# Kernel optimization log

Hardware: AMD Instinct MI355X
Metric: run time of the kernel (lower is better)

The kernel has to match this reference:

```python
import jax, jax.numpy as jnp
import numpy as np

N, E, C0, H, NC = 50000, 800000, 64, 64, 2500
NUM_LAYERS = 3


def setup_inputs() -> dict:
    key = jax.random.key(0)
    ks = jax.random.split(key, 16)
    inp = {}
    inp["x"] = jax.random.normal(ks[0], (N, C0), dtype=jnp.float32)
    inp["edge_index"] = jax.random.randint(ks[1], (2, E), 0, N, dtype=jnp.int64)
    inp["cluster"] = jax.random.randint(ks[2], (N,), 0, NC, dtype=jnp.int64)
    c = C0
    for i in range(NUM_LAYERS):
        inp[f"w1_{i}"] = jax.random.normal(ks[3 + 4 * i], (c, H), jnp.float32) / np.sqrt(c).astype(np.float32)
        inp[f"b1_{i}"] = jnp.zeros((H,), jnp.float32)
        inp[f"w2_{i}"] = jax.random.normal(ks[4 + 4 * i], (H, c), jnp.float32) / np.sqrt(H).astype(np.float32)
        inp[f"b2_{i}"] = jnp.zeros((c,), jnp.float32)
        c *= 2
    inp["n_clusters"] = NC
    return inp


def _glp(x, src, dst, w1, b1, w2, b2, num_nodes):
    # node encoder MLP: Linear -> ReLU -> Linear
    h = jnp.maximum(x @ w1 + b1, 0.0) @ w2 + b2  # [N, c]
    # message passing: gather at source, scatter-max at destination
    msg = h[src]  # [E, c]
    aggr = jax.ops.segment_max(msg, dst, num_segments=num_nodes)  # [N, c]
    # nodes with no incoming edges -> 0 (PyG fill for max aggregation)
    aggr = jnp.where(jnp.isfinite(aggr), aggr, 0.0)
    # update: concat(encoder_out, aggregated) -> channels double
    return jnp.concatenate([h, aggr], axis=1)


def reference(x, edge_index, cluster,
              w1_0, b1_0, w2_0, b2_0,
              w1_1, b1_1, w2_1, b2_1,
              w1_2, b1_2, w2_2, b2_2,
              n_clusters):
    num_nodes = x.shape[0]
    src, dst = edge_index[0], edge_index[1]
    params = [(w1_0, b1_0, w2_0, b2_0), (w1_1, b1_1, w2_1, b2_1), (w1_2, b1_2, w2_2, b2_2)]
    for (w1, b1, w2, b2) in params:
        x = _glp(x, src, dst, w1, b1, w2, b2, num_nodes)
    # cluster-wise max pool over polylines
    pooled = jax.ops.segment_max(x, cluster, num_segments=n_clusters)  # [NC, 512]
    pooled = jnp.where(jnp.isfinite(pooled), pooled, 0.0)
    # column-wise (dim=0) normalization as in the source
    out = pooled / (jnp.linalg.norm(pooled, axis=0) + 1e-6)
    return out
```

## Files before the change

### kernel.cpp

```cpp
#include <hip/hip_runtime.h>
#include <math.h>

typedef unsigned short bfu;
typedef __attribute__((ext_vector_type(8))) short bf16x8;
typedef __attribute__((ext_vector_type(16))) float f32x16;

__device__ __forceinline__ float b2f(bfu u) {
    unsigned int x = ((unsigned int)u) << 16;
    return __uint_as_float(x);
}
__device__ __forceinline__ bfu f2bf(float f) {
    unsigned int u = __float_as_uint(f);
    unsigned int r = (u + 0x7FFFu + ((u >> 16) & 1u)) >> 16;
    return (bfu)r;
}

struct InitArgs {
    int* deg; int N; int* cdeg; int NC; float* sumsq;
    const float* w[6]; bfu* whi[6]; bfu* wlo[6]; int K[6]; int Nw[6];
    const float* x0; bfu* xhi; bfu* xlo; int xtotal;
};

__global__ __launch_bounds__(256) void k_init(InitArgs a) {
    const int j = blockIdx.y;
    const int g0 = blockIdx.x * 256 + threadIdx.x;
    const int gs = gridDim.x * 256;
    if (j == 0) {
        for (int i = g0; i < a.N; i += gs) a.deg[i] = 0;
        for (int i = g0; i < a.NC; i += gs) a.cdeg[i] = 0;
        for (int i = g0; i < 512; i += gs) a.sumsq[i] = 0.f;
    } else if (j <= 6) {
        const int jj = j - 1;
        const int K = a.K[jj], Nw = a.Nw[jj];
        const int total = K * Nw;
        const float* w = a.w[jj];
        bfu* dhi = a.whi[jj];
        bfu* dlo = a.wlo[jj];
        for (int idx = g0; idx < total; idx += gs) {
            int k = idx / Nw, n = idx % Nw;
            float v = w[idx];
            bfu hi = f2bf(v);
            bfu lo = f2bf(v - b2f(hi));
            dhi[n * K + k] = hi;
            dlo[n * K + k] = lo;
        }
    } else {
        for (int i = g0; i * 4 < a.xtotal; i += gs) {
            int base = i * 4;
            float4 v = *(const float4*)&a.x0[base];
            ushort4 h, l;
            h.x = f2bf(v.x); l.x = f2bf(v.x - b2f(h.x));
            h.y = f2bf(v.y); l.y = f2bf(v.y - b2f(h.y));
            h.z = f2bf(v.z); l.z = f2bf(v.z - b2f(h.z));
            h.w = f2bf(v.w); l.w = f2bf(v.w - b2f(h.w));
            *(ushort4*)&a.xhi[base] = h;
            *(ushort4*)&a.xlo[base] = l;
        }
    }
}

__global__ void k_hist2(const int* __restrict__ dst, int E, int* __restrict__ deg,
                        const int* __restrict__ cluster, int N, int* __restrict__ cdeg) {
    int i = blockIdx.x * blockDim.x + threadIdx.x;
    if (i < E) atomicAdd(&deg[dst[i]], 1);
    if (i < N) atomicAdd(&cdeg[cluster[i]], 1);
}

__global__ __launch_bounds__(256) void k_scanA(const int* __restrict__ deg, int N,
                                               const int* __restrict__ cdeg, int NC,
                                               int* __restrict__ scn0, int* __restrict__ scn1,
                                               int* __restrict__ bsum0, int* __restrict__ bsum1) {
    __shared__ int part[256];
    const int seg = blockIdx.y;
    const int n = seg ? NC : N;
    const int* d = seg ? cdeg : deg;
    int* scn = seg ? scn1 : scn0;
    int* bs  = seg ? bsum1 : bsum0;
    const int b = blockIdx.x;
    if (b * 256 >= n) return;
    const int t = threadIdx.x;
    const int i = b * 256 + t;
    int v = (i < n) ? d[i] : 0;
    part[t] = v;
    __syncthreads();
#pragma unroll
    for (int off = 1; off < 256; off <<= 1) {
        int cv = part[t];
        int u = (t >= off) ? part[t - off] : 0;
        __syncthreads();
        part[t] = cv + u;
        __syncthreads();
    }
    if (i < n) scn[i] = part[t];
    if (t == 255) bs[b] = part[255];
}

__global__ __launch_bounds__(256) void k_scanC(const int* __restrict__ deg, int N,
                                               const int* __restrict__ cdeg, int NC,
                                               const int* __restrict__ scn0, const int* __restrict__ scn1,
                                               const int* __restrict__ bsum0, int nb0,
                                               const int* __restrict__ bsum1, int nb1,
                                               int* __restrict__ ptr0, int* __restrict__ cur0,
                                               int* __restrict__ ptr1, int* __restrict__ cur1) {
    __shared__ int part[256];
    const int seg = blockIdx.y;
    const int n = seg ? NC : N;
    const int nb = seg ? nb1 : nb0;
    const int* d = seg ? cdeg : deg;
    const int* scn = seg ? scn1 : scn0;
    const int* bsum = seg ? bsum1 : bsum0;
    int* ptr = seg ? ptr1 : ptr0;
    int* cur = seg ? cur1 : cur0;
    const int b = blockIdx.x;
    if (b * 256 >= n) return;
    const int t = threadIdx.x;
    int v = (t < nb) ? bsum[t] : 0;
    part[t] = v;
    __syncthreads();
#pragma unroll
    for (int off = 1; off < 256; off <<= 1) {
        int cv = part[t];
        int u = (t >= off) ? part[t - off] : 0;
        __syncthreads();
        part[t] = cv + u;
        __syncthreads();
    }
    const int boff = (b == 0) ? 0 : part[b - 1];
    const int i = b * 256 + t;
    if (i < n) {
        int e = boff + scn[i] - d[i];
        ptr[i] = e;
        cur[i] = e;
    }
    if (b == 0 && t == 0) ptr[n] = part[nb - 1];
}

__global__ void k_scatter2(const int* __restrict__ dst, const int* __restrict__ src, int E,
                           int* __restrict__ cur, int* __restrict__ colidx,
                           const int* __restrict__ cluster, int N,
                           int* __restrict__ ccur, int* __restrict__ cidx) {
    int i = blockIdx.x * blockDim.x + threadIdx.x;
    if (i < E) {
        int d = dst[i];
        int pos = atomicAdd(&cur[d], 1);
        colidx[pos] = src[i];
    }
    if (i < N) {
        int c = cluster[i];
        int pos = atomicAdd(&ccur[c], 1);
        cidx[pos] = i;
    }
}

__device__ __forceinline__ int swz(int row, int kb) {
    return (row * 128 + (kb ^ ((row & 7) << 4))) >> 1;
}

template <bool WLO>
__global__ __launch_bounds__(256) void k_layer(const bfu* __restrict__ Ahi, const bfu* __restrict__ Alo,
                                               const bfu* __restrict__ W1hi, const bfu* __restrict__ W1lo,
                                               const float* __restrict__ b1,
                                               const bfu* __restrict__ W2hi, const bfu* __restrict__ W2lo,
                                               const float* __restrict__ b2,
                                               bfu* __restrict__ Ohi, bfu* __restrict__ Olo,
                                               int M, int K, int Kzero, int Nw2, int OS) {
    __shared__ __align__(16) bfu As[2][128 * 64];
    __shared__ __align__(16) bfu Bs[2][64 * 64];
    const int tid = threadIdx.x;
    const int wave = tid >> 6, lane = tid & 63;
    const int m0 = blockIdx.x * 128;
    const int l31 = lane & 31;
    const int khalfb = (lane >> 5) * 16;
    const int arow = wave * 32 + l31;

    f32x16 acc0, acc1;
#pragma unroll
    for (int i = 0; i < 16; i++) { acc0[i] = 0.f; acc1[i] = 0.f; }

    for (int k0 = 0; k0 < K; k0 += 64) {
        const bool full3 = (k0 < Kzero);
#pragma unroll
        for (int i = 0; i < 4; i++) {
            int idx = i * 2048 + tid * 8;
            int row = idx >> 6;
            int ke = idx & 63;
            int gm = m0 + row; if (gm >= M) gm = M - 1;
            uint4 v = *(const uint4*)&Ahi[(size_t)gm * K + k0 + ke];
            *(uint4*)&As[0][swz(row, ke * 2)] = v;
        }
        if (full3) {
#pragma unroll
            for (int i = 0; i < 4; i++) {
                int idx = i * 2048 + tid * 8;
                int row = idx >> 6;
                int ke = idx & 63;
                int gm = m0 + row; if (gm >= M) gm = M - 1;
                uint4 v = *(const uint4*)&Alo[(size_t)gm * K + k0 + ke];
                *(uint4*)&As[1][swz(row, ke * 2)] = v;
            }
        }
#pragma unroll
        for (int p = 0; p < 2; p++) {
            const bfu* src = p ? W1lo : W1hi;
#pragma unroll
            for (int i = 0; i < 2; i++) {
                int idx = i * 2048 + tid * 8;
                int row = idx >> 6;
                int ke = idx & 63;
                uint4 v = *(const uint4*)&src[(size_t)row * K + k0 + ke];
                *(uint4*)&Bs[p][swz(row, ke * 2)] = v;
            }
        }
        __syncthreads();
#pragma unroll
        for (int s = 0; s < 4; s++) {
            int kb = s * 32 + khalfb;
            bf16x8 ah = *(const bf16x8*)&As[0][swz(arow, kb)];
            bf16x8 bh0 = *(const bf16x8*)&Bs[0][swz(l31, kb)];
            bf16x8 bl0 = *(const bf16x8*)&Bs[1][swz(l31, kb)];
            bf16x8 bh1 = *(const bf16x8*)&Bs[0][swz(32 + l31, kb)];
            bf16x8 bl1 = *(const bf16x8*)&Bs[1][swz(32 + l31, kb)];
            acc0 = __builtin_amdgcn_mfma_f32_32x32x16_bf16(ah, bh0, acc0, 0, 0, 0);
            acc0 = __builtin_amdgcn_mfma_f32_32x32x16_bf16(ah, bl0, acc0, 0, 0, 0);
            acc1 = __builtin_amdgcn_mfma_f32_32x32x16_bf16(ah, bh1, acc1, 0, 0, 0);
            acc1 = __builtin_amdgcn_mfma_f32_32x32x16_bf16(ah, bl1, acc1, 0, 0, 0);
            if (full3) {
                bf16x8 al = *(const bf16x8*)&As[1][swz(arow, kb)];
                acc0 = __builtin_amdgcn_mfma_f32_32x32x16_bf16(al, bh0, acc0, 0, 0, 0);
                acc1 = __builtin_amdgcn_mfma_f32_32x32x16_bf16(al, bh1, acc1, 0, 0, 0);
            }
        }
        __syncthreads();
    }

    {
        float bc0 = b1[l31];
        float bc1 = b1[32 + l31];
        const int rbase = wave * 32 + 4 * (lane >> 5);
#pragma unroll
        for (int r = 0; r < 16; r++) {
            int row = rbase + (r & 3) + 8 * (r >> 2);
            float t0 = fmaxf(acc0[r] + bc0, 0.f);
            float t1 = fmaxf(acc1[r] + bc1, 0.f);
            bfu h0 = f2bf(t0), h1 = f2bf(t1);
            bfu l0 = f2bf(t0 - b2f(h0)), l1 = f2bf(t1 - b2f(h1));
            As[0][swz(row, l31 * 2)] = h0;
            As[0][swz(row, (32 + l31) * 2)] = h1;
            As[1][swz(row, l31 * 2)] = l0;
            As[1][swz(row, (32 + l31) * 2)] = l1;
        }
    }

    for (int n0 = 0; n0 < Nw2; n0 += 64) {
        __syncthreads();
#pragma unroll
        for (int p = 0; p < 2; p++) {
            const bfu* src = p ? W2lo : W2hi;
#pragma unroll
            for (int i = 0; i < 2; i++) {
                int idx = i * 2048 + tid * 8;
                int row = idx >> 6;
                int ke = idx & 63;
                uint4 v = *(const uint4*)&src[(size_t)(n0 + row) * 64 + ke];
                *(uint4*)&Bs[p][swz(row, ke * 2)] = v;
            }
        }
        __syncthreads();
#pragma unroll
        for (int i = 0; i < 16; i++) { acc0[i] = 0.f; acc1[i] = 0.f; }
#pragma unroll
        for (int s = 0; s < 4; s++) {
            int kb = s * 32 + khalfb;
            bf16x8 th = *(const bf16x8*)&As[0][swz(arow, kb)];
            bf16x8 tl = *(const bf16x8*)&As[1][swz(arow, kb)];
            bf16x8 wh0 = *(const bf16x8*)&Bs[0][swz(l31, kb)];
            bf16x8 wl0 = *(const bf16x8*)&Bs[1][swz(l31, kb)];
            bf16x8 wh1 = *(const bf16x8*)&Bs[0][swz(32 + l31, kb)];
            bf16x8 wl1 = *(const bf16x8*)&Bs[1][swz(32 + l31, kb)];
            acc0 = __builtin_amdgcn_mfma_f32_32x32x16_bf16(th, wh0, acc0, 0, 0, 0);
            acc0 = __builtin_amdgcn_mfma_f32_32x32x16_bf16(th, wl0, acc0, 0, 0, 0);
            acc0 = __builtin_amdgcn_mfma_f32_32x32x16_bf16(tl, wh0, acc0, 0, 0, 0);
            acc1 = __builtin_amdgcn_mfma_f32_32x32x16_bf16(th, wh1, acc1, 0, 0, 0);
            acc1 = __builtin_amdgcn_mfma_f32_32x32x16_bf16(th, wl1, acc1, 0, 0, 0);
            acc1 = __builtin_amdgcn_mfma_f32_32x32x16_bf16(tl, wh1, acc1, 0, 0, 0);
        }
        float bc0 = b2[n0 + l31];
        float bc1 = b2[n0 + 32 + l31];
        const int rbase = m0 + wave * 32 + 4 * (lane >> 5);
#pragma unroll
        for (int r = 0; r < 16; r++) {
            int grow = rbase + (r & 3) + 8 * (r >> 2);
            if (grow < M) {
                float o0 = acc0[r] + bc0;
                float o1 = acc1[r] + bc1;
                bfu h0 = f2bf(o0), h1 = f2bf(o1);
                size_t base = (size_t)grow * OS + n0;
                Ohi[base + l31] = h0;
                Ohi[base + 32 + l31] = h1;
                if (WLO) {
                    Olo[base + l31] = f2bf(o0 - b2f(h0));
                    Olo[base + 32 + l31] = f2bf(o1 - b2f(h1));
                }
            }
        }
    }
}

template <int R>
__device__ __forceinline__ void gmax(const bfu* __restrict__ p, float* acc) {
    if (R == 4) {
        ushort4 v = *(const ushort4*)p;
        acc[0] = fmaxf(acc[0], b2f(v.x)); acc[1] = fmaxf(acc[1], b2f(v.y));
        acc[2] = fmaxf(acc[2], b2f(v.z)); acc[3] = fmaxf(acc[3], b2f(v.w));
    } else if (R == 2) {
        ushort2 v = *(const ushort2*)p;
        acc[0] = fmaxf(acc[0], b2f(v.x)); acc[1] = fmaxf(acc[1], b2f(v.y));
    } else {
        acc[0] = fmaxf(acc[0], b2f(*p));
    }
}

template <int R>
__global__ void k_agg(const bfu* __restrict__ hplane, bfu* __restrict__ whi,
                      const int* __restrict__ rowptr, const int* __restrict__ colidx,
                      int N, int stride) {
    const int wid = (blockIdx.x * blockDim.x + threadIdx.x) >> 6;
    const int lane = threadIdx.x & 63;
    if (wid >= N) return;
    const int beg = rowptr[wid], end = rowptr[wid + 1];
    const int ch = lane * R;

    float acc[R];
#pragma unroll
    for (int r = 0; r < R; r++) acc[r] = -INFINITY;

    int i = beg;
    for (; i + 8 <= end; i += 8) {
        int off[8];
#pragma unroll
        for (int u = 0; u < 8; u++) off[u] = colidx[i + u] * stride + ch;
#pragma unroll
        for (int u = 0; u < 8; u++) gmax<R>(hplane + off[u], acc);
    }
    for (; i + 2 <= end; i += 2) {
        int o0 = colidx[i] * stride + ch;
        int o1 = colidx[i + 1] * stride + ch;
        gmax<R>(hplane + o0, acc);
        gmax<R>(hplane + o1, acc);
    }
    if (i < end) gmax<R>(hplane + colidx[i] * stride + ch, acc);

    if (beg == end) {
#pragma unroll
        for (int r = 0; r < R; r++) acc[r] = 0.f;
    }
    int obase = wid * stride + 64 * R + ch;
#pragma unroll
    for (int r = 0; r < R; r++) whi[obase + r] = f2bf(acc[r]);
}

__global__ void k_pool(const bfu* __restrict__ xhi,
                       const int* __restrict__ cptr, const int* __restrict__ cidx,
                       float* __restrict__ pooled) {
    int cl = blockIdx.x;
    int tid = threadIdx.x;
    int beg = cptr[cl], end = cptr[cl + 1];
    float ax = -INFINITY, ay = -INFINITY;
    int i = beg;
    for (; i + 4 <= end; i += 4) {
        ushort2 h0 = *(const ushort2*)&xhi[cidx[i + 0] * 512 + tid * 2];
        ushort2 h1 = *(const ushort2*)&xhi[cidx[i + 1] * 512 + tid * 2];
        ushort2 h2 = *(const ushort2*)&xhi[cidx[i + 2] * 512 + tid * 2];
        ushort2 h3 = *(const ushort2*)&xhi[cidx[i + 3] * 512 + tid * 2];
        ax = fmaxf(ax, fmaxf(fmaxf(b2f(h0.x), b2f(h1.x)), fmaxf(b2f(h2.x), b2f(h3.x))));
        ay = fmaxf(ay, fmaxf(fmaxf(b2f(h0.y), b2f(h1.y)), fmaxf(b2f(h2.y), b2f(h3.y))));
    }
    for (; i < end; i++) {
        ushort2 h = *(const ushort2*)&xhi[cidx[i] * 512 + tid * 2];
        ax = fmaxf(ax, b2f(h.x)); ay = fmaxf(ay, b2f(h.y));
    }
    if (beg == end) { ax = 0.f; ay = 0.f; }
    float2 o; o.x = ax; o.y = ay;
    *(float2*)&pooled[(size_t)cl * 512 + tid * 2] = o;
}

__global__ void k_sumsq(const float* __restrict__ pooled, float* __restrict__ sumsq, int NC) {
    int tid = threadIdx.x;
    float ax = 0.f, ay = 0.f;
    for (int r = blockIdx.x; r < NC; r += gridDim.x) {
        float2 v = *(const float2*)&pooled[(size_t)r * 512 + tid * 2];
        ax += v.x * v.x; ay += v.y * v.y;
    }
    atomicAdd(&sumsq[tid * 2 + 0], ax);
    atomicAdd(&sumsq[tid * 2 + 1], ay);
}

__global__ void k_scale(const float* __restrict__ pooled, const float* __restrict__ sumsq,
                        float* __restrict__ out, int total) {
    int i = blockIdx.x * blockDim.x + threadIdx.x;
    int base = i * 4;
    if (base < total) {
        float4 v = *(const float4*)&pooled[base];
        int col = base & 511;
        v.x /= (sqrtf(sumsq[col + 0]) + 1e-6f);
        v.y /= (sqrtf(sumsq[col + 1]) + 1e-6f);
        v.z /= (sqrtf(sumsq[col + 2]) + 1e-6f);
        v.w /= (sqrtf(sumsq[col + 3]) + 1e-6f);
        *(float4*)&out[base] = v;
    }
}

extern "C" void kernel_launch(void* const* d_in, const int* in_sizes, int n_in,
                              void* d_out, int out_size, void* d_ws, size_t ws_size,
                              hipStream_t stream) {
    const float* x0      = (const float*)d_in[0];
    const int*   ei      = (const int*)d_in[1];
    const int*   cluster = (const int*)d_in[2];
    const float* w1_[3] = {(const float*)d_in[3], (const float*)d_in[7],  (const float*)d_in[11]};
    const float* b1_[3] = {(const float*)d_in[4], (const float*)d_in[8],  (const float*)d_in[12]};
    const float* w2_[3] = {(const float*)d_in[5], (const float*)d_in[9],  (const float*)d_in[13]};
    const float* b2_[3] = {(const float*)d_in[6], (const float*)d_in[10], (const float*)d_in[14]};

    const int N  = in_sizes[2];
    const int E  = in_sizes[1] / 2;
    const int NC = 2500;
    float* out = (float*)d_out;

    char* p = (char*)d_ws;
    auto alloc = [&](size_t bytes) -> char* {
        char* r = p;
        p += (bytes + 255) & ~(size_t)255;
        return r;
    };
    bfu* X0hi = (bfu*)alloc((size_t)N * 64 * 2);
    bfu* X0lo = (bfu*)alloc((size_t)N * 64 * 2);
    bfu* X1hi = (bfu*)alloc((size_t)N * 128 * 2);
    bfu* X1lo = (bfu*)alloc((size_t)N * 128 * 2);
    bfu* X2hi = (bfu*)alloc((size_t)N * 256 * 2);
    bfu* X2lo = (bfu*)alloc((size_t)N * 256 * 2);
    bfu* X3hi = (bfu*)alloc((size_t)N * 512 * 2);
    bfu* w1t_hi[3]; bfu* w1t_lo[3]; bfu* w2t_hi[3]; bfu* w2t_lo[3];
    const int Ks[3] = {64, 128, 256};
    for (int l = 0; l < 3; l++) {
        w1t_hi[l] = (bfu*)alloc((size_t)64 * Ks[l] * 2);
        w1t_lo[l] = (bfu*)alloc((size_t)64 * Ks[l] * 2);
        w2t_hi[l] = (bfu*)alloc((size_t)Ks[l] * 64 * 2);
        w2t_lo[l] = (bfu*)alloc((size_t)Ks[l] * 64 * 2);
    }
    float* pooled = (float*)alloc((size_t)NC * 512 * 4);
    float* sumsq  = (float*)alloc(512 * 4);
    int*   deg    = (int*)alloc((size_t)(N + 1) * 4);
    int*   rowptr = (int*)alloc((size_t)(N + 1) * 4);
    int*   cursor = (int*)alloc((size_t)(N + 1) * 4);
    int*   colidx = (int*)alloc((size_t)E * 4);
    int*   cdeg   = (int*)alloc((size_t)(NC + 1) * 4);
    int*   cptr   = (int*)alloc((size_t)(NC + 1) * 4);
    int*   ccur   = (int*)alloc((size_t)(NC + 1) * 4);
    int*   cidx   = (int*)alloc((size_t)N * 4);
    int*   scn0   = (int*)alloc((size_t)N * 4);
    int*   scn1   = (int*)alloc((size_t)NC * 4);
    int*   bsum0  = (int*)alloc(256 * 4);
    int*   bsum1  = (int*)alloc(256 * 4);

    const int* src = ei;
    const int* dst = ei + E;

    InitArgs ia;
    ia.deg = deg; ia.N = N; ia.cdeg = cdeg; ia.NC = NC; ia.sumsq = sumsq;
    for (int l = 0; l < 3; l++) {
        ia.w[2 * l]     = w1_[l]; ia.whi[2 * l]     = w1t_hi[l]; ia.wlo[2 * l]     = w1t_lo[l];
        ia.K[2 * l]     = Ks[l];  ia.Nw[2 * l]      = 64;
        ia.w[2 * l + 1] = w2_[l]; ia.whi[2 * l + 1] = w2t_hi[l]; ia.wlo[2 * l + 1] = w2t_lo[l];
        ia.K[2 * l + 1] = 64;     ia.Nw[2 * l + 1]  = Ks[l];
    }
    ia.x0 = x0; ia.xhi = X0hi; ia.xlo = X0lo; ia.xtotal = N * 64;
    k_init<<<dim3(128, 8), 256, 0, stream>>>(ia);

    k_hist2<<<(E + 255) / 256, 256, 0, stream>>>(dst, E, deg, cluster, N, cdeg);

    const int nb0 = (N + 255) / 256;
    const int nb1 = (NC + 255) / 256;
    k_scanA<<<dim3(nb0, 2), 256, 0, stream>>>(deg, N, cdeg, NC, scn0, scn1, bsum0, bsum1);
    k_scanC<<<dim3(nb0, 2), 256, 0, stream>>>(deg, N, cdeg, NC, scn0, scn1, bsum0, nb0, bsum1, nb1,
                                              rowptr, cursor, cptr, ccur);

    k_scatter2<<<(E + 255) / 256, 256, 0, stream>>>(dst, src, E, cursor, colidx,
                                                    cluster, N, ccur, cidx);

    const int Mt = (N + 127) / 128;
    const int aggBlocks = (N * 64 + 255) / 256;

    k_layer<true><<<Mt, 256, 0, stream>>>(X0hi, X0lo, w1t_hi[0], w1t_lo[0], b1_[0],
                                          w2t_hi[0], w2t_lo[0], b2_[0], X1hi, X1lo,
                                          N, 64, 64, 64, 128);
    k_agg<1><<<aggBlocks, 256, 0, stream>>>(X1hi, X1hi, rowptr, colidx, N, 128);

    k_layer<true><<<Mt, 256, 0, stream>>>(X1hi, X1lo, w1t_hi[1], w1t_lo[1], b1_[1],
                                          w2t_hi[1], w2t_lo[1], b2_[1], X2hi, X2lo,
                                          N, 128, 64, 128, 256);
    k_agg<2><<<aggBlocks, 256, 0, stream>>>(X2hi, X2hi, rowptr, colidx, N, 256);

    k_layer<false><<<Mt, 256, 0, stream>>>(X2hi, X2lo, w1t_hi[2], w1t_lo[2], b1_[2],
                                           w2t_hi[2], w2t_lo[2], b2_[2], X3hi, nullptr,
                                           N, 256, 128, 256, 512);
    k_agg<4><<<aggBlocks, 256, 0, stream>>>(X3hi, X3hi, rowptr, colidx, N, 512);

    k_pool<<<NC, 256, 0, stream>>>(X3hi, cptr, cidx, pooled);
    k_sumsq<<<64, 256, 0, stream>>>(pooled, sumsq, NC);
    k_scale<<<(out_size / 4 + 255) / 256, 256, 0, stream>>>(pooled, sumsq, out, out_size);
}
```

Baseline: 303.5 us.

## Split each wavefront across several edges with 16-byte gathers in aggregation

Rewrites the scatter-max aggregation kernel so each wavefront breaks into sub-groups that each handle a different incoming edge. Every lane loads 8 bf16 channels (16 bytes) at once, and partial maxima are combined across sub-groups with xor shuffles. The aim is fewer, wider memory transactions and more parallel gathers per node, since average degree is about 16. The cost is the shuffle reduction, idle lanes on low-degree nodes, and duplicated loads in the tail.

```diff
diff --git a/kernel.cpp b/kernel.cpp
--- a/kernel.cpp
+++ b/kernel.cpp
@@ -306,57 +306,76 @@
     }
 }
 
-template <int R>
-__device__ __forceinline__ void gmax(const bfu* __restrict__ p, float* acc) {
-    if (R == 4) {
-        ushort4 v = *(const ushort4*)p;
-        acc[0] = fmaxf(acc[0], b2f(v.x)); acc[1] = fmaxf(acc[1], b2f(v.y));
-        acc[2] = fmaxf(acc[2], b2f(v.z)); acc[3] = fmaxf(acc[3], b2f(v.w));
-    } else if (R == 2) {
-        ushort2 v = *(const ushort2*)p;
-        acc[0] = fmaxf(acc[0], b2f(v.x)); acc[1] = fmaxf(acc[1], b2f(v.y));
-    } else {
-        acc[0] = fmaxf(acc[0], b2f(*p));
-    }
-}
-
-template <int R>
-__global__ void k_agg(const bfu* __restrict__ hplane, bfu* __restrict__ whi,
-                      const int* __restrict__ rowptr, const int* __restrict__ colidx,
-                      int N, int stride) {
+__device__ __forceinline__ void gmax8(const bfu* __restrict__ p, float* acc) {
+    uint4 v = *(const uint4*)p;
+    acc[0] = fmaxf(acc[0], __uint_as_float(v.x << 16));
+    acc[1] = fmaxf(acc[1], __uint_as_float(v.x & 0xffff0000u));
+    acc[2] = fmaxf(acc[2], __uint_as_float(v.y << 16));
+    acc[3] = fmaxf(acc[3], __uint_as_float(v.y & 0xffff0000u));
+    acc[4] = fmaxf(acc[4], __uint_as_float(v.z << 16));
+    acc[5] = fmaxf(acc[5], __uint_as_float(v.z & 0xffff0000u));
+    acc[6] = fmaxf(acc[6], __uint_as_float(v.w << 16));
+    acc[7] = fmaxf(acc[7], __uint_as_float(v.w & 0xffff0000u));
+}
+
+template <int LPR, int STRIDE>
+__global__ void k_aggw(const bfu* __restrict__ hplane, bfu* __restrict__ whi,
+                       const int* __restrict__ rowptr, const int* __restrict__ colidx,
+                       int N) {
     const int wid = (blockIdx.x * blockDim.x + threadIdx.x) >> 6;
     const int lane = threadIdx.x & 63;
     if (wid >= N) return;
     const int beg = rowptr[wid], end = rowptr[wid + 1];
-    const int ch = lane * R;
-
-    float acc[R];
-#pragma unroll
-    for (int r = 0; r < R; r++) acc[r] = -INFINITY;
+    constexpr int EPL = 64 / LPR;
+    const int sub = lane >> ( LPR == 32 ? 5 : (LPR == 16 ? 4 : 3) );
+    const int ll  = lane & (LPR - 1);
+    const int ch  = ll * 8;
+
+    float acc[8];
+#pragma unroll
+    for (int r = 0; r < 8; r++) acc[r] = -INFINITY;
 
     int i = beg;
-    for (; i + 8 <= end; i += 8) {
+    for (; i + 8 * EPL <= end; i += 8 * EPL) {
         int off[8];
 #pragma unroll
-        for (int u = 0; u < 8; u++) off[u] = colidx[i + u] * stride + ch;
-#pragma unroll
-        for (int u = 0; u < 8; u++) gmax<R>(hplane + off[u], acc);
-    }
-    for (; i + 2 <= end; i += 2) {
-        int o0 = colidx[i] * stride + ch;
-        int o1 = colidx[i + 1] * stride + ch;
-        gmax<R>(hplane + o0, acc);
-        gmax<R>(hplane + o1, acc);
-    }
-    if (i < end) gmax<R>(hplane + colidx[i] * stride + ch, acc);
+        for (int u = 0; u < 8; u++) off[u] = colidx[i + u * EPL + sub] * STRIDE + ch;
+#pragma unroll
+        for (int u = 0; u < 8; u++) gmax8(hplane + off[u], acc);
+    }
+    for (; i + 2 * EPL <= end; i += 2 * EPL) {
+        int o0 = colidx[i + sub] * STRIDE + ch;
+        int o1 = colidx[i + EPL + sub] * STRIDE + ch;
+        gmax8(hplane + o0, acc);
+        gmax8(hplane + o1, acc);
+    }
+    for (; i + EPL <= end; i += EPL) {
+        gmax8(hplane + colidx[i + sub] * STRIDE + ch, acc);
+    }
+    if (i < end) {
+        int r = end - i;
+        int e = i + (sub < r ? sub : r - 1);
+        gmax8(hplane + colidx[e] * STRIDE + ch, acc);
+    }
+
+#pragma unroll
+    for (int m = LPR; m < 64; m <<= 1) {
+#pragma unroll
+        for (int r = 0; r < 8; r++) acc[r] = fmaxf(acc[r], __shfl_xor(acc[r], m, 64));
+    }
 
     if (beg == end) {
 #pragma unroll
-        for (int r = 0; r < R; r++) acc[r] = 0.f;
-    }
-    int obase = wid * stride + 64 * R + ch;
-#pragma unroll
-    for (int r = 0; r < R; r++) whi[obase + r] = f2bf(acc[r]);
+        for (int r = 0; r < 8; r++) acc[r] = 0.f;
+    }
+    if (sub == 0) {
+        ushort4 w0, w1;
+        w0.x = f2bf(acc[0]); w0.y = f2bf(acc[1]); w0.z = f2bf(acc[2]); w0.w = f2bf(acc[3]);
+        w1.x = f2bf(acc[4]); w1.y = f2bf(acc[5]); w1.z = f2bf(acc[6]); w1.w = f2bf(acc[7]);
+        bfu* q = whi + (size_t)wid * STRIDE + STRIDE / 2 + ch;
+        *(ushort4*)q = w0;
+        *(ushort4*)(q + 4) = w1;
+    }
 }
 
 __global__ void k_pool(const bfu* __restrict__ xhi,
@@ -493,17 +512,17 @@
     k_layer<true><<<Mt, 256, 0, stream>>>(X0hi, X0lo, w1t_hi[0], w1t_lo[0], b1_[0],
                                           w2t_hi[0], w2t_lo[0], b2_[0], X1hi, X1lo,
                                           N, 64, 64, 64, 128);
-    k_agg<1><<<aggBlocks, 256, 0, stream>>>(X1hi, X1hi, rowptr, colidx, N, 128);
+    k_aggw<8, 128><<<aggBlocks, 256, 0, stream>>>(X1hi, X1hi, rowptr, colidx, N);
 
     k_layer<true><<<Mt, 256, 0, stream>>>(X1hi, X1lo, w1t_hi[1], w1t_lo[1], b1_[1],
                                           w2t_hi[1], w2t_lo[1], b2_[1], X2hi, X2lo,
                                           N, 128, 64, 128, 256);
-    k_agg<2><<<aggBlocks, 256, 0, stream>>>(X2hi, X2hi, rowptr, colidx, N, 256);
+    k_aggw<16, 256><<<aggBlocks, 256, 0, stream>>>(X2hi, X2hi, rowptr, colidx, N);
 
     k_layer<false><<<Mt, 256, 0, stream>>>(X2hi, X2lo, w1t_hi[2], w1t_lo[2], b1_[2],
                                            w2t_hi[2], w2t_lo[2], b2_[2], X3hi, nullptr,
                                            N, 256, 128, 256, 512);
-    k_agg<4><<<aggBlocks, 256, 0, stream>>>(X3hi, X3hi, rowptr, colidx, N, 512);
+    k_aggw<32, 512><<<aggBlocks, 256, 0, stream>>>(X3hi, X3hi, rowptr, colidx, N);
 
     k_pool<<<NC, 256, 0, stream>>>(X3hi, cptr, cidx, pooled);
     k_sumsq<<<64, 256, 0, stream>>>(pooled, sumsq, NC);
```

New measurement: 309.2 us. About the same (+1.9%).

## Halve MLP row tile to 64 and split output columns across waves

Applied to the files above, without the earlier changes.

The fused two-layer MLP kernel now processes 64 rows per block instead of 128. The four waves form a 2x2 grid (row half by column half), so each wave holds one 32x32 accumulator instead of two. This halves LDS use for the A tile and the accumulator registers, and doubles the number of blocks, which should raise occupancy and parallelism over the 50k rows. In exchange, the weight tiles are loaded from global memory twice as often per row, and each wave has half as many MFMAs in flight.

```diff
diff --git a/kernel.cpp b/kernel.cpp
--- a/kernel.cpp
+++ b/kernel.cpp
@@ -164,23 +164,24 @@
                                                const float* __restrict__ b2,
                                                bfu* __restrict__ Ohi, bfu* __restrict__ Olo,
                                                int M, int K, int Kzero, int Nw2, int OS) {
-    __shared__ __align__(16) bfu As[2][128 * 64];
+    __shared__ __align__(16) bfu As[2][64 * 64];
     __shared__ __align__(16) bfu Bs[2][64 * 64];
     const int tid = threadIdx.x;
     const int wave = tid >> 6, lane = tid & 63;
-    const int m0 = blockIdx.x * 128;
+    const int m0 = blockIdx.x * 64;
     const int l31 = lane & 31;
     const int khalfb = (lane >> 5) * 16;
-    const int arow = wave * 32 + l31;
-
-    f32x16 acc0, acc1;
-#pragma unroll
-    for (int i = 0; i < 16; i++) { acc0[i] = 0.f; acc1[i] = 0.f; }
+    const int arow = (wave & 1) * 32 + l31;
+    const int cbase = (wave >> 1) * 32;
+
+    f32x16 acc;
+#pragma unroll
+    for (int i = 0; i < 16; i++) acc[i] = 0.f;
 
     for (int k0 = 0; k0 < K; k0 += 64) {
         const bool full3 = (k0 < Kzero);
 #pragma unroll
-        for (int i = 0; i < 4; i++) {
+        for (int i = 0; i < 2; i++) {
             int idx = i * 2048 + tid * 8;
             int row = idx >> 6;
             int ke = idx & 63;
@@ -190,7 +191,7 @@
         }
         if (full3) {
 #pragma unroll
-            for (int i = 0; i < 4; i++) {
+            for (int i = 0; i < 2; i++) {
                 int idx = i * 2048 + tid * 8;
                 int row = idx >> 6;
                 int ke = idx & 63;
@@ -216,38 +217,29 @@
         for (int s = 0; s < 4; s++) {
             int kb = s * 32 + khalfb;
             bf16x8 ah = *(const bf16x8*)&As[0][swz(arow, kb)];
-            bf16x8 bh0 = *(const bf16x8*)&Bs[0][swz(l31, kb)];
-            bf16x8 bl0 = *(const bf16x8*)&Bs[1][swz(l31, kb)];
-            bf16x8 bh1 = *(const bf16x8*)&Bs[0][swz(32 + l31, kb)];
-            bf16x8 bl1 = *(const bf16x8*)&Bs[1][swz(32 + l31, kb)];
-            acc0 = __builtin_amdgcn_mfma_f32_32x32x16_bf16(ah, bh0, acc0, 0, 0, 0);
-            acc0 = __builtin_amdgcn_mfma_f32_32x32x16_bf16(ah, bl0, acc0, 0, 0, 0);
-            acc1 = __builtin_amdgcn_mfma_f32_32x32x16_bf16(ah, bh1, acc1, 0, 0, 0);
-            acc1 = __builtin_amdgcn_mfma_f32_32x32x16_bf16(ah, bl1, acc1, 0, 0, 0);
+            bf16x8 bh = *(const bf16x8*)&Bs[0][swz(cbase + l31, kb)];
+            bf16x8 bl = *(const bf16x8*)&Bs[1][swz(cbase + l31, kb)];
+            acc = __builtin_amdgcn_mfma_f32_32x32x16_bf16(ah, bh, acc, 0, 0, 0);
+            acc = __builtin_amdgcn_mfma_f32_32x32x16_bf16(ah, bl, acc, 0, 0, 0);
             if (full3) {
                 bf16x8 al = *(const bf16x8*)&As[1][swz(arow, kb)];
-                acc0 = __builtin_amdgcn_mfma_f32_32x32x16_bf16(al, bh0, acc0, 0, 0, 0);
-                acc1 = __builtin_amdgcn_mfma_f32_32x32x16_bf16(al, bh1, acc1, 0, 0, 0);
+                acc = __builtin_amdgcn_mfma_f32_32x32x16_bf16(al, bh, acc, 0, 0, 0);
             }
         }
         __syncthreads();
     }
 
     {
-        float bc0 = b1[l31];
-        float bc1 = b1[32 + l31];
-        const int rbase = wave * 32 + 4 * (lane >> 5);
+        float bc = b1[cbase + l31];
+        const int rbase = (wave & 1) * 32 + 4 * (lane >> 5);
 #pragma unroll
         for (int r = 0; r < 16; r++) {
             int row = rbase + (r & 3) + 8 * (r >> 2);
-            float t0 = fmaxf(acc0[r] + bc0, 0.f);
-            float t1 = fmaxf(acc1[r] + bc1, 0.f);
-            bfu h0 = f2bf(t0), h1 = f2bf(t1);
-            bfu l0 = f2bf(t0 - b2f(h0)), l1 = f2bf(t1 - b2f(h1));
-            As[0][swz(row, l31 * 2)] = h0;
-            As[0][swz(row, (32 + l31) * 2)] = h1;
-            As[1][swz(row, l31 * 2)] = l0;
-            As[1][swz(row, (32 + l31) * 2)] = l1;
+            float t0 = fmaxf(acc[r] + bc, 0.f);
+            bfu h0 = f2bf(t0);
+            bfu l0 = f2bf(t0 - b2f(h0));
+            As[0][swz(row, (cbase + l31) * 2)] = h0;
+            As[1][swz(row, (cbase + l31) * 2)] = l0;
         }
     }
 
@@ -267,39 +259,30 @@
         }
         __syncthreads();
 #pragma unroll
-        for (int i = 0; i < 16; i++) { acc0[i] = 0.f; acc1[i] = 0.f; }
+        for (int i = 0; i < 16; i++) acc[i] = 0.f;
 #pragma unroll
         for (int s = 0; s < 4; s++) {
             int kb = s * 32 + khalfb;
             bf16x8 th = *(const bf16x8*)&As[0][swz(arow, kb)];
             bf16x8 tl = *(const bf16x8*)&As[1][swz(arow, kb)];
-            bf16x8 wh0 = *(const bf16x8*)&Bs[0][swz(l31, kb)];
-            bf16x8 wl0 = *(const bf16x8*)&Bs[1][swz(l31, kb)];
-            bf16x8 wh1 = *(const bf16x8*)&Bs[0][swz(32 + l31, kb)];
-            bf16x8 wl1 = *(const bf16x8*)&Bs[1][swz(32 + l31, kb)];
-            acc0 = __builtin_amdgcn_mfma_f32_32x32x16_bf16(th, wh0, acc0, 0, 0, 0);
-            acc0 = __builtin_amdgcn_mfma_f32_32x32x16_bf16(th, wl0, acc0, 0, 0, 0);
-            acc0 = __builtin_amdgcn_mfma_f32_32x32x16_bf16(tl, wh0, acc0, 0, 0, 0);
-            acc1 = __builtin_amdgcn_mfma_f32_32x32x16_bf16(th, wh1, acc1, 0, 0, 0);
-            acc1 = __builtin_amdgcn_mfma_f32_32x32x16_bf16(th, wl1, acc1, 0, 0, 0);
-            acc1 = __builtin_amdgcn_mfma_f32_32x32x16_bf16(tl, wh1, acc1, 0, 0, 0);
-        }
-        float bc0 = b2[n0 + l31];
-        float bc1 = b2[n0 + 32 + l31];
-        const int rbase = m0 + wave * 32 + 4 * (lane >> 5);
+            bf16x8 wh = *(const bf16x8*)&Bs[0][swz(cbase + l31, kb)];
+            bf16x8 wl = *(const bf16x8*)&Bs[1][swz(cbase + l31, kb)];
+            acc = __builtin_amdgcn_mfma_f32_32x32x16_bf16(th, wh, acc, 0, 0, 0);
+            acc = __builtin_amdgcn_mfma_f32_32x32x16_bf16(th, wl, acc, 0, 0, 0);
+            acc = __builtin_amdgcn_mfma_f32_32x32x16_bf16(tl, wh, acc, 0, 0, 0);
+        }
+        float bc = b2[n0 + cbase + l31];
+        const int rbase = m0 + (wave & 1) * 32 + 4 * (lane >> 5);
 #pragma unroll
         for (int r = 0; r < 16; r++) {
             int grow = rbase + (r & 3) + 8 * (r >> 2);
             if (grow < M) {
-                float o0 = acc0[r] + bc0;
-                float o1 = acc1[r] + bc1;
-                bfu h0 = f2bf(o0), h1 = f2bf(o1);
-                size_t base = (size_t)grow * OS + n0;
+                float o0 = acc[r] + bc;
+                bfu h0 = f2bf(o0);
+                size_t base = (size_t)grow * OS + n0 + cbase;
                 Ohi[base + l31] = h0;
-                Ohi[base + 32 + l31] = h1;
                 if (WLO) {
                     Olo[base + l31] = f2bf(o0 - b2f(h0));
-                    Olo[base + 32 + l31] = f2bf(o1 - b2f(h1));
                 }
             }
         }
@@ -487,7 +470,7 @@
     k_scatter2<<<(E + 255) / 256, 256, 0, stream>>>(dst, src, E, cursor, colidx,
                                                     cluster, N, ccur, cidx);
 
-    const int Mt = (N + 127) / 128;
+    const int Mt = (N + 63) / 64;
     const int aggBlocks = (N * 64 + 255) / 256;
 
     k_layer<true><<<Mt, 256, 0, stream>>>(X0hi, X0lo, w1t_hi[0], w1t_lo[0], b1_[0],
```

Measured after the change: 307.1 us. No clear change (+1.2%).
